# Optimization experiments

Measured on AMD Instinct MI355X. Metric: run time of the kernel, lower is better.

## Reference

```python
import jax, jax.numpy as jnp
import numpy as np

S_DIM = 16
NUM_HEADS = 4
DIM_VEC = S_DIM * (S_DIM + 1) // 2  # 136
HEAD_DIM = DIM_VEC // NUM_HEADS     # 34
EPS = 1e-8

# row-major lower-triangle indices (matches torch.tril_indices ordering)
TRIL_R, TRIL_C = np.tril_indices(S_DIM)


def log_eig(X):
    w, V = jnp.linalg.eigh(X)
    w = jnp.clip(w, EPS, None)
    return jnp.einsum('...ij,...j,...kj->...ik', V, jnp.log(w), V)


def exp_eig(X):
    w, V = jnp.linalg.eigh(X)
    return jnp.einsum('...ij,...j,...kj->...ik', V, jnp.exp(w), V)


def mha(x, in_w, in_b, out_w, out_b):
    # torch nn.MultiheadAttention (batch_first, eval mode / no dropout)
    B, L, d = x.shape
    qkv = x @ in_w.T + in_b                       # [B,L,3d]
    q, k, v = jnp.split(qkv, 3, axis=-1)
    def heads(t):
        return t.reshape(B, L, NUM_HEADS, HEAD_DIM).transpose(0, 2, 1, 3)
    q, k, v = heads(q), heads(k), heads(v)        # [B,H,L,hd]
    scores = jnp.einsum('bhqd,bhkd->bhqk', q, k) / np.sqrt(HEAD_DIM).astype(np.float32)
    attn = jax.nn.softmax(scores, axis=-1)
    o = jnp.einsum('bhqk,bhkd->bhqd', attn, v)
    o = o.transpose(0, 2, 1, 3).reshape(B, L, d)
    return o @ out_w.T + out_b


def setup_inputs() -> dict:
    key = jax.random.key(0)
    k0, k1, k2 = jax.random.split(key, 3)
    B, L = 16, 1024
    A = jax.random.normal(k0, (B, L, S_DIM, S_DIM), jnp.float32)
    # SPD input: A A^T / s + 0.1 I
    S = A @ jnp.swapaxes(A, -1, -2) / S_DIM + 0.1 * jnp.eye(S_DIM, dtype=jnp.float32)
    d = DIM_VEC
    scale = 1.0 / np.sqrt(d)
    in_proj_w = jax.random.uniform(k1, (3 * d, d), jnp.float32, -scale, scale)
    in_proj_b = jnp.zeros((3 * d,), jnp.float32)
    out_proj_w = jax.random.uniform(k2, (d, d), jnp.float32, -scale, scale)
    out_proj_b = jnp.zeros((d,), jnp.float32)
    return {"S": S, "in_proj_w": in_proj_w, "in_proj_b": in_proj_b,
            "out_proj_w": out_proj_w, "out_proj_b": out_proj_b}


def reference(S, in_proj_w, in_proj_b, out_proj_w, out_proj_b):
    B, L, s, _ = S.shape
    logs = log_eig(S)                                  # [B,L,s,s]
    vec_in = logs[..., TRIL_R, TRIL_C]                 # [B,L,dim_vec]
    vec_out = mha(vec_in, in_proj_w, in_proj_b, out_proj_w, out_proj_b) + vec_in
    sym = jnp.zeros((B, L, s, s), S.dtype).at[..., TRIL_R, TRIL_C].set(vec_out)
    diag = jnp.diagonal(sym, axis1=-2, axis2=-1)       # [B,L,s]
    sym = sym + jnp.swapaxes(sym, -1, -2) - jnp.eye(s, dtype=S.dtype) * diag[..., None, :]
    return exp_eig(sym)
```

## Files before the change

kernel.cpp:

```cpp
#include <hip/hip_runtime.h>
#include <math.h>

#define B_SZ 16
#define L_SZ 1024
#define NMAT (B_SZ * L_SZ)
#define DIMV 136
#define QKVD 408
#define HD 34
#define NH 4
#define NSWEEP 5

typedef __attribute__((ext_vector_type(8))) short short8;
typedef __attribute__((ext_vector_type(16))) float f32x16;
union F8 { short8 s; uint32_t u[4]; };

struct S3 { uint32_t h, m, l; };
__device__ __forceinline__ S3 split3(float x) {
  S3 r;
  uint32_t xb = __float_as_uint(x);
  r.h = xb & 0xffff0000u;
  float rr = x - __uint_as_float(r.h);
  r.m = __float_as_uint(rr) & 0xffff0000u;
  float r2 = rr - __uint_as_float(r.m);
  r.l = __float_as_uint(r2) & 0xffff0000u;
  return r;
}
__device__ __forceinline__ uint32_t pkb(uint32_t a, uint32_t b) { return (a >> 16) | b; }

__device__ __forceinline__ float sel16(const float a[16], int j) {
  float p0 = (j & 1) ? a[1] : a[0];
  float p1 = (j & 1) ? a[3] : a[2];
  float p2 = (j & 1) ? a[5] : a[4];
  float p3 = (j & 1) ? a[7] : a[6];
  float p4 = (j & 1) ? a[9] : a[8];
  float p5 = (j & 1) ? a[11] : a[10];
  float p6 = (j & 1) ? a[13] : a[12];
  float p7 = (j & 1) ? a[15] : a[14];
  float q0 = (j & 2) ? p1 : p0;
  float q1 = (j & 2) ? p3 : p2;
  float q2 = (j & 2) ? p5 : p4;
  float q3 = (j & 2) ? p7 : p6;
  float r0 = (j & 4) ? q1 : q0;
  float r1 = (j & 4) ? q3 : q2;
  return (j & 8) ? r1 : r0;
}

__device__ __forceinline__ void jacobi16_reg(float a[16], float v[16], float& diag,
                                             const int lane) {
  const int sub = lane & 15;
  const int gbase = lane & 48;
  for (int sweep = 0; sweep < NSWEEP; ++sweep) {
#pragma unroll
    for (int r = 0; r < 15; ++r) {
      int partner;
      if (sub == 15) partner = r;
      else {
        int d = sub - r; if (d < 0) d += 15;
        if (d == 0) partner = 15;
        else if (d <= 7) { partner = r - d; if (partner < 0) partner += 15; }
        else { partner = r + 15 - d; if (partner >= 15) partner -= 15; }
      }
      const int plane = gbase | partner;
      float oa[16], ov[16];
#pragma unroll
      for (int i = 0; i < 16; ++i) oa[i] = __shfl(a[i], plane);
#pragma unroll
      for (int i = 0; i < 16; ++i) ov[i] = __shfl(v[i], plane);
      const float diag_o = __shfl(diag, plane);
      const bool amP = sub < partner;
      const float app = amP ? diag : diag_o;
      const float aqq = amP ? diag_o : diag;
      const float apq_loc = sel16(a, partner);
      const int pl = gbase | (amP ? sub : partner);
      const float apq = __shfl(apq_loc, pl);
      float c, s, t;
      {
        float theta = (aqq - app) / (2.f * apq);
        float tt = 1.f / (fabsf(theta) + sqrtf(fmaf(theta, theta, 1.f)));
        tt = (theta < 0.f) ? -tt : tt;
        t = (fabsf(apq) < 1e-30f) ? 0.f : tt;
        c = rsqrtf(fmaf(t, t, 1.f));
        s = t * c;
      }
      const float sgn = amP ? -s : s;
#pragma unroll
      for (int i = 0; i < 16; ++i) {
        a[i] = fmaf(sgn, oa[i], c * a[i]);
        v[i] = fmaf(sgn, ov[i], c * v[i]);
      }
      const float cc = c * c, ss2 = s * s, cs2 = 2.f * c * s;
      const float dp = fmaf(cc, app, fmaf(ss2, aqq, -cs2 * apq));
      const float dq = fmaf(ss2, app, fmaf(cc, aqq, cs2 * apq));
      diag = amP ? dp : dq;
#pragma unroll
      for (int k = 0; k < 8; ++k) {
        const int owner = (k == 0) ? r : (r + k) % 15;
        const float tk = __shfl(t, gbase | owner);
        const float ck = rsqrtf(fmaf(tk, tk, 1.f));
        const float sk = tk * ck;
        int pk, qk;
        if (k == 0) { pk = r; qk = 15; }
        else {
          const int u = (r + k) % 15, w = (r + 15 - k) % 15;
          pk = u < w ? u : w; qk = u < w ? w : u;
        }
        float tp = a[pk], tq = a[qk];
        a[pk] = fmaf(-sk, tq, ck * tp);
        a[qk] = fmaf(sk, tp, ck * tq);
      }
    }
  }
}

__global__ __launch_bounds__(256) void k1_logvec(const float* __restrict__ S, float* __restrict__ vec) {
  __shared__ float Vld[16][272];
  __shared__ float lwld[16][16];
  const int tid = threadIdx.x;
  const int lane = tid & 63;
  const int mloc = tid >> 4;
  const int sub = tid & 15;
  const int mat = blockIdx.x * 16 + mloc;
  float a[16], v[16], diag = 0.f;
  const float* Sp = S + (size_t)mat * 256;
#pragma unroll
  for (int i = 0; i < 16; ++i) {
    a[i] = Sp[i * 16 + sub];
    v[i] = (i == sub) ? 1.f : 0.f;
    if (i == sub) diag = a[i];
  }
  jacobi16_reg(a, v, diag, lane);
  float* Vc = &Vld[mloc][0];
#pragma unroll
  for (int i = 0; i < 16; ++i) Vc[sub * 17 + i] = v[i];
  lwld[mloc][sub] = __logf(fmaxf(diag, 1e-8f));
  __syncthreads();
  for (int idx = sub; idx < DIMV; idx += 16) {
    int rr = (int)((sqrtf(8.f * (float)idx + 1.f) - 1.f) * 0.5f);
    while ((rr + 1) * (rr + 2) / 2 <= idx) ++rr;
    while (rr * (rr + 1) / 2 > idx) --rr;
    const int ccol = idx - rr * (rr + 1) / 2;
    float acc = 0.f;
#pragma unroll
    for (int j = 0; j < 16; ++j)
      acc += lwld[mloc][j] * Vc[j * 17 + rr] * Vc[j * 17 + ccol];
    vec[(size_t)idx * NMAT + mat] = acc;
  }
}

__global__ __launch_bounds__(256) void k2_qkv(const float* __restrict__ X, const float* __restrict__ W,
                                              const float* __restrict__ bias, float* __restrict__ Y) {
  const int r0 = blockIdx.x * 512 + threadIdx.x * 2;
  const int n0 = blockIdx.y * 17;
  float accx[17], accy[17];
#pragma unroll
  for (int c = 0; c < 17; ++c) { const float bv = bias[n0 + c]; accx[c] = bv; accy[c] = bv; }
  for (int k = 0; k < DIMV; ++k) {
    const float2 xv = *(const float2*)&X[(size_t)k * NMAT + r0];
#pragma unroll
    for (int c = 0; c < 17; ++c) {
      const float wv = W[(size_t)(n0 + c) * DIMV + k];
      accx[c] = fmaf(wv, xv.x, accx[c]);
      accy[c] = fmaf(wv, xv.y, accy[c]);
    }
  }
  const int b = r0 >> 10, lrow = r0 & 1023;
#pragma unroll
  for (int c = 0; c < 17; ++c) {
    const int n = n0 + c;
    const int p = n / DIMV, rr = n - p * DIMV;
    const int hh = rr / HD, dd = rr - hh * HD;
    *(float2*)&Y[(((size_t)(p * 64 + b * NH + hh)) * HD + dd) * L_SZ + lrow] =
        make_float2(accx[c], accy[c]);
  }
}

__global__ __launch_bounds__(256) void k3_attn(const float* __restrict__ QKV, float* __restrict__ Oout) {
  __shared__ __align__(16) uint32_t Kh[6 * 32 * 4], Km[6 * 32 * 4], Kl[6 * 32 * 4];
  __shared__ __align__(16) uint16_t VTh[4 * 64 * 8], VTm[4 * 64 * 8], VTl[4 * 64 * 8];
  const int tid = threadIdx.x;
  const int lane = tid & 63;
  const int w = tid >> 6;
  const int bh = blockIdx.x;
  const int head = bh & 3;
  const int b = bh >> 2;
  const int qrl = lane & 31;
  const int hh = lane >> 5;
  const int row = blockIdx.y * 128 + w * 32 + qrl;
  const float* __restrict__ Qp = QKV + ((size_t)(0 * 64 + bh)) * HD * L_SZ;
  const float* __restrict__ Kp = QKV + ((size_t)(1 * 64 + bh)) * HD * L_SZ;
  const float* __restrict__ Vp = QKV + ((size_t)(2 * 64 + bh)) * HD * L_SZ;
  const float scale = 0.1714985851425088f;

  for (int i = tid; i < 6 * 32 * 4; i += 256) { Kh[i] = 0; Km[i] = 0; Kl[i] = 0; }
  for (int i = tid; i < 4 * 64 * 8; i += 256) { VTh[i] = 0; VTm[i] = 0; VTl[i] = 0; }

  F8 qfh[3], qfm[3], qfl[3];
#pragma unroll
  for (int c = 0; c < 3; ++c) {
#pragma unroll
    for (int e2 = 0; e2 < 4; ++e2) {
      const int kd = c * 16 + hh * 8 + 2 * e2;
      float x = 0.f, y = 0.f;
      if (kd < HD) {
        x = Qp[(size_t)kd * L_SZ + row] * scale;
        y = Qp[(size_t)(kd + 1) * L_SZ + row] * scale;
      }
      S3 sx = split3(x), sy = split3(y);
      qfh[c].u[e2] = pkb(sx.h, sy.h);
      qfm[c].u[e2] = pkb(sx.m, sy.m);
      qfl[c].u[e2] = pkb(sx.l, sy.l);
    }
  }

  f32x16 o0, o1;
#pragma unroll
  for (int i = 0; i < 16; ++i) { o0[i] = 0.f; o1[i] = 0.f; }
  float mrun = -3.0e38f, lsum = 0.f;

  for (int t = 0; t < 32; ++t) {
    __syncthreads();
    for (int u = tid; u < 1088; u += 256) {
      const bool isK = u < 544;
      const int e = isK ? u : u - 544;
      const int key = e & 31;
      const int j = e >> 5;
      const float* __restrict__ P = isK ? Kp : Vp;
      const size_t base = (size_t)(t * 32 + key);
      const float x = P[(size_t)(2 * j) * L_SZ + base];
      const float y = P[(size_t)(2 * j + 1) * L_SZ + base];
      const S3 sx = split3(x), sy = split3(y);
      if (isK) {
        const int di = ((j >> 2) * 32 + key) * 4 + (j & 3);
        Kh[di] = pkb(sx.h, sy.h); Km[di] = pkb(sx.m, sy.m); Kl[di] = pkb(sx.l, sy.l);
      } else {
        const int b0 = ((key >> 3) * 64 + 2 * j) * 8 + (key & 7);
        VTh[b0] = (uint16_t)(sx.h >> 16); VTm[b0] = (uint16_t)(sx.m >> 16); VTl[b0] = (uint16_t)(sx.l >> 16);
        VTh[b0 + 8] = (uint16_t)(sy.h >> 16); VTm[b0 + 8] = (uint16_t)(sy.m >> 16); VTl[b0 + 8] = (uint16_t)(sy.l >> 16);
      }
    }
    __syncthreads();

    f32x16 s;
#pragma unroll
    for (int i = 0; i < 16; ++i) s[i] = 0.f;
#pragma unroll
    for (int c = 0; c < 3; ++c) {
      F8 ah, am, al;
      const int kidx = ((c * 2 + hh) * 32 + qrl) * 4;
      ah.s = *(const short8*)&Kh[kidx];
      am.s = *(const short8*)&Km[kidx];
      al.s = *(const short8*)&Kl[kidx];
      s = __builtin_amdgcn_mfma_f32_32x32x16_bf16(ah.s, qfh[c].s, s, 0, 0, 0);
      s = __builtin_amdgcn_mfma_f32_32x32x16_bf16(ah.s, qfm[c].s, s, 0, 0, 0);
      s = __builtin_amdgcn_mfma_f32_32x32x16_bf16(am.s, qfh[c].s, s, 0, 0, 0);
      s = __builtin_amdgcn_mfma_f32_32x32x16_bf16(ah.s, qfl[c].s, s, 0, 0, 0);
      s = __builtin_amdgcn_mfma_f32_32x32x16_bf16(am.s, qfm[c].s, s, 0, 0, 0);
      s = __builtin_amdgcn_mfma_f32_32x32x16_bf16(al.s, qfh[c].s, s, 0, 0, 0);
    }

    float mymax = s[0];
#pragma unroll
    for (int e = 1; e < 16; ++e) mymax = fmaxf(mymax, s[e]);
    const float pmax = fmaxf(mymax, __shfl_xor(mymax, 32));
    const float mn = fmaxf(mrun, pmax);
    const float corr = __expf(mrun - mn);
    mrun = mn;
    float p[16]; float ps = 0.f;
#pragma unroll
    for (int e = 0; e < 16; ++e) { p[e] = __expf(s[e] - mn); ps += p[e]; }
    ps += __shfl_xor(ps, 32);
    lsum = lsum * corr + ps;
    o0 *= corr; o1 *= corr;

    uint32_t uo[3][8], po[3][8];
#pragma unroll
    for (int g = 0; g < 8; ++g) {
      const S3 s0 = split3(p[2 * g]), s1 = split3(p[2 * g + 1]);
      uo[0][g] = pkb(s0.h, s1.h); uo[1][g] = pkb(s0.m, s1.m); uo[2][g] = pkb(s0.l, s1.l);
    }
#pragma unroll
    for (int sp = 0; sp < 3; ++sp)
#pragma unroll
      for (int g = 0; g < 8; ++g) po[sp][g] = (uint32_t)__shfl_xor((int)uo[sp][g], 32);
    F8 pf[3][2];
#pragma unroll
    for (int sp = 0; sp < 3; ++sp) {
      pf[sp][0].u[0] = hh ? po[sp][2] : uo[sp][0];
      pf[sp][0].u[1] = hh ? po[sp][3] : uo[sp][1];
      pf[sp][0].u[2] = hh ? uo[sp][2] : po[sp][0];
      pf[sp][0].u[3] = hh ? uo[sp][3] : po[sp][1];
      pf[sp][1].u[0] = hh ? po[sp][6] : uo[sp][4];
      pf[sp][1].u[1] = hh ? po[sp][7] : uo[sp][5];
      pf[sp][1].u[2] = hh ? uo[sp][6] : po[sp][4];
      pf[sp][1].u[3] = hh ? uo[sp][7] : po[sp][5];
    }

#pragma unroll
    for (int dt = 0; dt < 2; ++dt) {
#pragma unroll
      for (int kc = 0; kc < 2; ++kc) {
        const int vb = ((kc * 2 + hh) * 64 + dt * 32 + qrl) * 8;
        F8 vh2, vm2, vl2;
        vh2.s = *(const short8*)&VTh[vb];
        vm2.s = *(const short8*)&VTm[vb];
        vl2.s = *(const short8*)&VTl[vb];
        f32x16 oa = dt ? o1 : o0;
        oa = __builtin_amdgcn_mfma_f32_32x32x16_bf16(vh2.s, pf[0][kc].s, oa, 0, 0, 0);
        oa = __builtin_amdgcn_mfma_f32_32x32x16_bf16(vh2.s, pf[1][kc].s, oa, 0, 0, 0);
        oa = __builtin_amdgcn_mfma_f32_32x32x16_bf16(vm2.s, pf[0][kc].s, oa, 0, 0, 0);
        oa = __builtin_amdgcn_mfma_f32_32x32x16_bf16(vh2.s, pf[2][kc].s, oa, 0, 0, 0);
        oa = __builtin_amdgcn_mfma_f32_32x32x16_bf16(vm2.s, pf[1][kc].s, oa, 0, 0, 0);
        oa = __builtin_amdgcn_mfma_f32_32x32x16_bf16(vl2.s, pf[0][kc].s, oa, 0, 0, 0);
        if (dt) o1 = oa; else o0 = oa;
      }
    }
  }

  const float inv = 1.f / lsum;
  const int rowG = b * L_SZ + row;
#pragma unroll
  for (int dt = 0; dt < 2; ++dt) {
#pragma unroll
    for (int rq = 0; rq < 4; ++rq) {
#pragma unroll
      for (int j = 0; j < 4; ++j) {
        const int d = dt * 32 + 8 * rq + 4 * hh + j;
        if (d < HD) {
          const float val = (dt ? o1[rq * 4 + j] : o0[rq * 4 + j]) * inv;
          Oout[(size_t)(head * HD + d) * NMAT + rowG] = val;
        }
      }
    }
  }
}

__global__ __launch_bounds__(256) void k4_outproj(const float* __restrict__ X, const float* __restrict__ W,
                                                  const float* __restrict__ bias, const float* __restrict__ resid,
                                                  float* __restrict__ Y) {
  const int r0 = blockIdx.x * 512 + threadIdx.x * 2;
  const int n0 = blockIdx.y * 17;
  float accx[17], accy[17];
#pragma unroll
  for (int c = 0; c < 17; ++c) { const float bv = bias[n0 + c]; accx[c] = bv; accy[c] = bv; }
  for (int k = 0; k < DIMV; ++k) {
    const float2 xv = *(const float2*)&X[(size_t)k * NMAT + r0];
#pragma unroll
    for (int c = 0; c < 17; ++c) {
      const float wv = W[(size_t)(n0 + c) * DIMV + k];
      accx[c] = fmaf(wv, xv.x, accx[c]);
      accy[c] = fmaf(wv, xv.y, accy[c]);
    }
  }
#pragma unroll
  for (int c = 0; c < 17; ++c) {
    const float2 rv = *(const float2*)&resid[(size_t)(n0 + c) * NMAT + r0];
    *(float2*)&Y[(size_t)(n0 + c) * NMAT + r0] = make_float2(accx[c] + rv.x, accy[c] + rv.y);
  }
}

__global__ __launch_bounds__(256) void k5_expm(const float* __restrict__ vecOut, float* __restrict__ out) {
  __shared__ float Vld[16][272];
  __shared__ float eld[16][16];
  const int tid = threadIdx.x;
  const int lane = tid & 63;
  const int mloc = tid >> 4;
  const int sub = tid & 15;
  const int mat = blockIdx.x * 16 + mloc;
  float a[16], v[16], diag = 0.f;
#pragma unroll
  for (int i = 0; i < 16; ++i) {
    const int rr = i > sub ? i : sub;
    const int cc = i + sub - rr;
    a[i] = vecOut[(size_t)(rr * (rr + 1) / 2 + cc) * NMAT + mat];
    v[i] = (i == sub) ? 1.f : 0.f;
    if (i == sub) diag = a[i];
  }
  jacobi16_reg(a, v, diag, lane);
  float* Vc = &Vld[mloc][0];
#pragma unroll
  for (int i = 0; i < 16; ++i) Vc[sub * 17 + i] = v[i];
  eld[mloc][sub] = __expf(diag);
  __syncthreads();
  float u[16];
#pragma unroll
  for (int j = 0; j < 16; ++j) u[j] = eld[mloc][j] * Vc[j * 17 + sub];
#pragma unroll
  for (int i = 0; i < 16; ++i) {
    float acc = 0.f;
#pragma unroll
    for (int j = 0; j < 16; ++j) acc = fmaf(u[j], Vc[j * 17 + i], acc);
    out[(size_t)mat * 256 + i * 16 + sub] = acc;
  }
}

extern "C" void kernel_launch(void* const* d_in, const int* in_sizes, int n_in,
                              void* d_out, int out_size, void* d_ws, size_t ws_size,
                              hipStream_t stream) {
  const float* S     = (const float*)d_in[0];
  const float* in_w  = (const float*)d_in[1];
  const float* in_b  = (const float*)d_in[2];
  const float* out_w = (const float*)d_in[3];
  const float* out_b = (const float*)d_in[4];
  float* out = (float*)d_out;
  float* ws = (float*)d_ws;
  float* vec_in  = ws;
  float* qkv     = vec_in + (size_t)NMAT * DIMV;
  float* attn    = qkv    + (size_t)NMAT * QKVD;
  float* vec_out = attn   + (size_t)NMAT * DIMV;

  k1_logvec <<<dim3(NMAT / 16),      dim3(256), 0, stream>>>(S, vec_in);
  k2_qkv    <<<dim3(NMAT / 512, 24), dim3(256), 0, stream>>>(vec_in, in_w, in_b, qkv);
  k3_attn   <<<dim3(64, 8),          dim3(256), 0, stream>>>(qkv, attn);
  k4_outproj<<<dim3(NMAT / 512, 8),  dim3(256), 0, stream>>>(attn, out_w, out_b, vec_in, vec_out);
  k5_expm   <<<dim3(NMAT / 16),      dim3(256), 0, stream>>>(vec_out, out);
}
```

Baseline: 636.9 us.

## Replace Jacobi eigen-based matrix exponential with scaled Taylor and squaring on MFMA

The final matrix exponential no longer runs a Jacobi eigendecomposition. It now uses a scaling-and-squaring scheme with a degree-6 Taylor polynomial in Horner form. The matrix products run on bf16 MFMA instructions with a three-way bf16 split (six MFMAs per product) to approximate fp32 accuracy, and each wavefront handles two matrices packed into one 32x32 tile. This aims to remove the costly iterative Jacobi sweeps, at the cost of accuracy that depends on the norm-based scaling and on the truncated Taylor series.

```diff
diff --git a/kernel.cpp b/kernel.cpp
--- a/kernel.cpp
+++ b/kernel.cpp
@@ -358,39 +358,107 @@
   }
 }
 
+__device__ __forceinline__ void frag_from_acc(const f32x16& acc, bool hiM, int h, float F[8]) {
+  float uq[8], rq[8];
+#pragma unroll
+  for (int j = 0; j < 8; ++j) uq[j] = hiM ? acc[8 + j] : acc[j];
+#pragma unroll
+  for (int j = 0; j < 8; ++j) rq[j] = __shfl_xor(uq[j], 32);
+  F[0] = h ? rq[4] : uq[0];
+  F[1] = h ? rq[5] : uq[1];
+  F[2] = h ? rq[6] : uq[2];
+  F[3] = h ? rq[7] : uq[3];
+  F[4] = h ? uq[4] : rq[0];
+  F[5] = h ? uq[5] : rq[1];
+  F[6] = h ? uq[6] : rq[2];
+  F[7] = h ? uq[7] : rq[3];
+}
+
+__device__ __forceinline__ void split_frag(const float F[8], F8& Xh, F8& Xm, F8& Xl) {
+#pragma unroll
+  for (int e2 = 0; e2 < 4; ++e2) {
+    const S3 a = split3(F[2 * e2]), b = split3(F[2 * e2 + 1]);
+    Xh.u[e2] = pkb(a.h, b.h);
+    Xm.u[e2] = pkb(a.m, b.m);
+    Xl.u[e2] = pkb(a.l, b.l);
+  }
+}
+
+__device__ __forceinline__ f32x16 mm6(const F8& Ah, const F8& Am, const F8& Al,
+                                      const F8& Bh, const F8& Bm, const F8& Bl) {
+  f32x16 acc;
+#pragma unroll
+  for (int i = 0; i < 16; ++i) acc[i] = 0.f;
+  acc = __builtin_amdgcn_mfma_f32_32x32x16_bf16(Ah.s, Bh.s, acc, 0, 0, 0);
+  acc = __builtin_amdgcn_mfma_f32_32x32x16_bf16(Ah.s, Bm.s, acc, 0, 0, 0);
+  acc = __builtin_amdgcn_mfma_f32_32x32x16_bf16(Am.s, Bh.s, acc, 0, 0, 0);
+  acc = __builtin_amdgcn_mfma_f32_32x32x16_bf16(Ah.s, Bl.s, acc, 0, 0, 0);
+  acc = __builtin_amdgcn_mfma_f32_32x32x16_bf16(Am.s, Bm.s, acc, 0, 0, 0);
+  acc = __builtin_amdgcn_mfma_f32_32x32x16_bf16(Al.s, Bh.s, acc, 0, 0, 0);
+  return acc;
+}
+
 __global__ __launch_bounds__(256) void k5_expm(const float* __restrict__ vecOut, float* __restrict__ out) {
-  __shared__ float Vld[16][272];
-  __shared__ float eld[16][16];
   const int tid = threadIdx.x;
   const int lane = tid & 63;
-  const int mloc = tid >> 4;
-  const int sub = tid & 15;
-  const int mat = blockIdx.x * 16 + mloc;
-  float a[16], v[16], diag = 0.f;
+  const int wv = tid >> 6;
+  const int h = lane >> 5;
+  const int x = lane & 31;
+  const int xp = x & 15;
+  const bool hiM = (x >> 4) != 0;
+  const int mat = blockIdx.x * 8 + wv * 2 + (x >> 4);
+
+  float m[16];
+  float nrm = 0.f;
 #pragma unroll
   for (int i = 0; i < 16; ++i) {
-    const int rr = i > sub ? i : sub;
-    const int cc = i + sub - rr;
-    a[i] = vecOut[(size_t)(rr * (rr + 1) / 2 + cc) * NMAT + mat];
-    v[i] = (i == sub) ? 1.f : 0.f;
-    if (i == sub) diag = a[i];
-  }
-  jacobi16_reg(a, v, diag, lane);
-  float* Vc = &Vld[mloc][0];
-#pragma unroll
-  for (int i = 0; i < 16; ++i) Vc[sub * 17 + i] = v[i];
-  eld[mloc][sub] = __expf(diag);
-  __syncthreads();
-  float u[16];
-#pragma unroll
-  for (int j = 0; j < 16; ++j) u[j] = eld[mloc][j] * Vc[j * 17 + sub];
-#pragma unroll
-  for (int i = 0; i < 16; ++i) {
-    float acc = 0.f;
-#pragma unroll
-    for (int j = 0; j < 16; ++j) acc = fmaf(u[j], Vc[j * 17 + i], acc);
-    out[(size_t)mat * 256 + i * 16 + sub] = acc;
-  }
+    const int rr = i > xp ? i : xp;
+    const int cc = i + xp - rr;
+    m[i] = vecOut[(size_t)(rr * (rr + 1) / 2 + cc) * NMAT + mat];
+    nrm += fabsf(m[i]);
+  }
+#pragma unroll
+  for (int off = 1; off <= 32; off <<= 1) nrm = fmaxf(nrm, __shfl_xor(nrm, off));
+  int ex;
+  frexpf(nrm, &ex);
+  int sq = ex + 2;
+  sq = sq < 0 ? 0 : (sq > 15 ? 15 : sq);
+  const float scl = __int_as_float((uint32_t)(127 - sq) << 23);
+
+  float bF[8];
+#pragma unroll
+  for (int e = 0; e < 8; ++e) bF[e] = (h ? m[8 + e] : m[e]) * scl;
+  F8 Bh, Bm, Bl;
+  split_frag(bF, Bh, Bm, Bl);
+
+  float tF[8];
+#pragma unroll
+  for (int e = 0; e < 8; ++e)
+    tF[e] = fmaf(bF[e], 1.f / 6.f, (xp == (h ? 8 : 0) + e) ? 1.f : 0.f);
+  F8 Th, Tm, Tl;
+  split_frag(tF, Th, Tm, Tl);
+
+  const float invc[5] = {0.2f, 0.25f, 1.f / 3.f, 0.5f, 1.f};
+#pragma unroll
+  for (int kk = 0; kk < 5; ++kk) {
+    f32x16 acc = mm6(Bh, Bm, Bl, Th, Tm, Tl);
+    float F[8];
+    frag_from_acc(acc, hiM, h, F);
+#pragma unroll
+    for (int e = 0; e < 8; ++e)
+      tF[e] = fmaf(F[e], invc[kk], (xp == (h ? 8 : 0) + e) ? 1.f : 0.f);
+    split_frag(tF, Th, Tm, Tl);
+  }
+
+  for (int i = 0; i < sq; ++i) {
+    f32x16 acc = mm6(Th, Tm, Tl, Th, Tm, Tl);
+    frag_from_acc(acc, hiM, h, tF);
+    split_frag(tF, Th, Tm, Tl);
+  }
+
+  float* op = out + (size_t)mat * 256 + xp;
+#pragma unroll
+  for (int e = 0; e < 8; ++e) op[(h * 8 + e) * 16] = tF[e];
 }
 
 extern "C" void kernel_launch(void* const* d_in, const int* in_sizes, int n_in,
@@ -412,5 +480,5 @@
   k2_qkv    <<<dim3(NMAT / 512, 24), dim3(256), 0, stream>>>(vec_in, in_w, in_b, qkv);
   k3_attn   <<<dim3(64, 8),          dim3(256), 0, stream>>>(qkv, attn);
   k4_outproj<<<dim3(NMAT / 512, 8),  dim3(256), 0, stream>>>(attn, out_w, out_b, vec_in, vec_out);
-  k5_expm   <<<dim3(NMAT / 16),      dim3(256), 0, stream>>>(vec_out, out);
-}
+  k5_expm   <<<dim3(NMAT / 8),       dim3(256), 0, stream>>>(vec_out, out);
+}
```

After: 515.9 us. 1.23x faster.
